# Kernel optimization log

Hardware: AMD Instinct MI355X
Metric: run time of the kernel (lower is better)

The kernel has to match this reference:

```python
import jax, jax.numpy as jnp
import numpy as np

N_NODES, N_EDGES, N_FEAT, N_HID = 50000, 800000, 512, 64


def gcn_conv(x, W, b, src, dst, ew):
    """PyG-style GCNConv: linear -> symmetric-normalized aggregation with self-loops -> +bias."""
    N = x.shape[0]
    h = x @ W  # [N, H]
    # degree includes the implicit self-loop of weight 1 (PyG gcn_norm default)
    deg = jax.ops.segment_sum(ew, dst, num_segments=N) + 1.0
    dinv = jax.lax.rsqrt(deg)  # deg^{-1/2}
    coef = dinv[src] * ew * dinv[dst]  # [E]
    out = jax.ops.segment_sum(h[src] * coef[:, None], dst, num_segments=N)
    out = out + h * (dinv * dinv)[:, None]  # self-loop contribution
    return out + b


def setup_inputs() -> dict:
    key = jax.random.key(0)
    k0, k1, k2, k3 = jax.random.split(key, 4)
    x = jax.random.normal(k0, (N_NODES, N_FEAT), dtype=jnp.float32)
    edge_index = jax.random.randint(k1, (2, N_EDGES), 0, N_NODES, dtype=jnp.int64)
    edge_weight = jnp.ones((N_EDGES,), dtype=jnp.float32)
    W1 = jax.random.normal(k2, (N_FEAT, N_HID), dtype=jnp.float32) * (1.0 / np.sqrt(N_FEAT))
    b1 = jnp.zeros((N_HID,), dtype=jnp.float32)
    W2 = jax.random.normal(k3, (N_HID, N_HID), dtype=jnp.float32) * (1.0 / np.sqrt(N_HID))
    b2 = jnp.zeros((N_HID,), dtype=jnp.float32)
    return {"x": x, "edge_index": edge_index, "edge_weight": edge_weight,
            "W1": W1, "b1": b1, "W2": W2, "b2": b2}


def reference(x, edge_index, edge_weight, W1, b1, W2, b2):
    # Grace.forward -> GCN_body.forward in eval mode (no dropout, no LN)
    src, dst = edge_index[0], edge_index[1]
    h = jax.nn.relu(gcn_conv(x, W1, b1, src, dst, edge_weight))
    h = jax.nn.relu(gcn_conv(h, W2, b2, src, dst, edge_weight))
    return h
```

## Files before the change

### kernel.cpp

```cpp
#include <hip/hip_runtime.h>
#include <hip/hip_bf16.h>

typedef __bf16 bf16x8 __attribute__((ext_vector_type(8)));
typedef float  f32x4  __attribute__((ext_vector_type(4)));

#define RNODES 64
#define ROWCAP 1792
#define NB 128
#define MAXNR 1024
#define FIXB 256

__device__ __forceinline__ float bf_lo(unsigned int v) { return __uint_as_float(v << 16); }
__device__ __forceinline__ float bf_hi(unsigned int v) { return __uint_as_float(v & 0xFFFF0000u); }

__device__ __forceinline__ void pack_one(const void* __restrict__ W, int f16,
                                         __hip_bfloat16* __restrict__ Wp, int K, int t) {
    int j  = t & 7;
    int l  = (t >> 3) & 63;
    int nt = (t >> 9) & 3;
    int kt = t >> 11;
    int k = kt * 32 + (l >> 4) * 8 + j;
    int n = nt * 16 + (l & 15);
    size_t gi = (size_t)k * 64 + n;
    Wp[t] = f16 ? ((const __hip_bfloat16*)W)[gi]
                : __float2bfloat16(((const float*)W)[gi]);
}

__global__ void setup_kernel(const unsigned int* __restrict__ ew_raw,
                             const unsigned int* __restrict__ ei_raw,
                             const void* __restrict__ W1, const void* __restrict__ W2,
                             int* __restrict__ flags,
                             __hip_bfloat16* __restrict__ W1p, __hip_bfloat16* __restrict__ W2p,
                             int F, int H) {
    int f16 = (ew_raw[0] == 0x3F803F80u) ? 1 : 0;
    if (blockIdx.x == 0 && threadIdx.x == 0) {
        flags[0] = f16;
        flags[1] = ((ei_raw[1] | ei_raw[3] | ei_raw[5] | ei_raw[7]) == 0u) ? 1 : 0;
        flags[2] = 0;
        flags[3] = 0;
        flags[4] = 1;
    }
    int t = blockIdx.x * 256 + threadIdx.x;
    if (t < F * 64)            pack_one(W1, f16, W1p, F, t);
    else if (t < (F + H) * 64) pack_one(W2, f16, W2p, H, t - F * 64);
}

__device__ __forceinline__ void gemm_body(const void* __restrict__ A,
                                          const __hip_bfloat16* __restrict__ Wp,
                                          int a_f32, __hip_bfloat16* __restrict__ out,
                                          int M, int K, int gt) {
    int wid  = gt >> 6;
    int lane = gt & 63;
    if (wid >= (M >> 4)) return;
    int row0 = wid << 4;
    int quad = lane >> 4, mr = lane & 15;
    const bf16x8* bp = (const bf16x8*)((const void*)Wp) + lane;

    f32x4 acc[4];
    #pragma unroll
    for (int nt = 0; nt < 4; ++nt) acc[nt] = (f32x4){0.f, 0.f, 0.f, 0.f};

    int KT = K >> 5;
    const __hip_bfloat16* ab    = (const __hip_bfloat16*)A + (size_t)(row0 + mr) * K + quad * 8;
    const float*          af32p = (const float*)A + (size_t)(row0 + mr) * K + quad * 8;

    int kt = 0;
    for (; kt + 8 <= KT; kt += 8) {
        bf16x8 af[8];
        if (a_f32) {
            #pragma unroll
            for (int u = 0; u < 8; ++u) {
                const float* ar = af32p + (kt + u) * 32;
                #pragma unroll
                for (int j = 0; j < 8; ++j) af[u][j] = (__bf16)ar[j];
            }
        } else {
            #pragma unroll
            for (int u = 0; u < 8; ++u)
                af[u] = ((const bf16x8*)((const void*)(ab + (kt + u) * 32)))[0];
        }
        #pragma unroll
        for (int u = 0; u < 8; ++u)
            #pragma unroll
            for (int nt = 0; nt < 4; ++nt)
                acc[nt] = __builtin_amdgcn_mfma_f32_16x16x32_bf16(
                              af[u], bp[((kt + u) * 4 + nt) * 64], acc[nt], 0, 0, 0);
    }
    for (; kt < KT; ++kt) {
        bf16x8 af;
        if (a_f32) {
            const float* ar = af32p + kt * 32;
            #pragma unroll
            for (int j = 0; j < 8; ++j) af[j] = (__bf16)ar[j];
        } else {
            af = ((const bf16x8*)((const void*)(ab + kt * 32)))[0];
        }
        #pragma unroll
        for (int nt = 0; nt < 4; ++nt)
            acc[nt] = __builtin_amdgcn_mfma_f32_16x16x32_bf16(
                          af, bp[(kt * 4 + nt) * 64], acc[nt], 0, 0, 0);
    }

    __hip_bfloat16* o = out + (size_t)row0 * 64;
    #pragma unroll
    for (int nt = 0; nt < 4; ++nt)
        #pragma unroll
        for (int rr = 0; rr < 4; ++rr)
            o[(size_t)(quad * 4 + rr) * 64 + nt * 16 + mr] = __float2bfloat16(acc[nt][rr]);
}

__global__ void gemm_mfma(const void* __restrict__ A, const __hip_bfloat16* __restrict__ Wp,
                          const int* __restrict__ flags, __hip_bfloat16* __restrict__ out,
                          int M, int K, int a_mode) {
    int gt = blockIdx.x * blockDim.x + threadIdx.x;
    int a_f32 = (a_mode == 2) && (flags[0] == 0);
    gemm_body(A, Wp, a_f32, out, M, K, gt);
}

__global__ void bgp1_kernel(const void* __restrict__ A, const __hip_bfloat16* __restrict__ Wp,
                            __hip_bfloat16* __restrict__ outH,
                            const int* __restrict__ ei, const void* __restrict__ ew,
                            int* __restrict__ flags,
                            int* __restrict__ blockhist, unsigned int* __restrict__ pkstage,
                            int M, int K, int E, int NR, int gblocks) {
    if ((int)blockIdx.x < gblocks) {
        gemm_body(A, Wp, flags[0] == 0, outH, M, K, blockIdx.x * 256 + threadIdx.x);
        return;
    }
    __shared__ int hist[MAXNR];
    int b = blockIdx.x - gblocks, tid = threadIdx.x;
    for (int i = tid; i < NR; i += 256) hist[i] = 0;
    __syncthreads();
    int f16 = flags[0], i64 = flags[1];

    int nw = f16 ? (E >> 1) : E;
    unsigned int expect = f16 ? 0x3F803F80u : 0x3F800000u;
    int wchunk = (nw + NB - 1) / NB;
    int w0 = b * wchunk, w1 = w0 + wchunk; if (w1 > nw) w1 = nw;
    const unsigned int* ewr = (const unsigned int*)ew;
    unsigned int bad = 0;
    for (int i = w0 + tid; i < w1; i += 256) bad |= (ewr[i] ^ expect);
    if (bad) flags[4] = 0;

    int chunk = (E + NB - 1) / NB;
    int e0 = b * chunk, e1 = e0 + chunk; if (e1 > E) e1 = E;
    for (int e = e0 + tid; e < e1; e += 256) {
        int s, d;
        if (i64) { s = ei[2LL * e]; d = ei[2LL * ((long long)E + e)]; }
        else     { s = ei[e];       d = ei[E + e]; }
        int r = d >> 6;
        atomicAdd(&hist[r], 1);
        pkstage[e] = ((unsigned int)r << 22) | ((unsigned int)s << 6) | (unsigned int)(d & 63);
    }
    __syncthreads();
    for (int i = tid; i < NR; i += 256) blockhist[b * NR + i] = hist[i];
}

__device__ __forceinline__ void check_body(const void* __restrict__ A, const void* __restrict__ W,
                                           int* __restrict__ flags,
                                           const __hip_bfloat16* __restrict__ out,
                                           int N, int K, int a_mode, int fidx, int bid) {
    __shared__ float xs[4 * 512];
    int f16 = flags[0];
    int a_f32 = (a_mode == 2) && (f16 == 0);
    int tid = threadIdx.x;
    int total = 4 * K;
    for (int t = tid; t < total; t += 256) {
        int nn = t / K, kk = t - nn * K;
        int n = (int)(((long long)(bid * 4 + nn) * 977) % N);
        long long gi = (long long)n * K + kk;
        float v = a_f32 ? (float)(__bf16)(((const float*)A)[gi])
                        : __bfloat162float(((const __hip_bfloat16*)A)[gi]);
        xs[t] = v;
    }
    __syncthreads();
    int j = tid & 63, local = tid >> 6;
    int n = (int)(((long long)(bid * 4 + local) * 977) % N);
    const float* xr = xs + local * K;
    float acc = 0.f;
    if (f16) {
        const __hip_bfloat16* Wb = (const __hip_bfloat16*)W;
        #pragma unroll 8
        for (int k = 0; k < K; ++k) acc += xr[k] * __bfloat162float(Wb[(long long)k * 64 + j]);
    } else {
        const float* Wf = (const float*)W;
        #pragma unroll 8
        for (int k = 0; k < K; ++k) acc += xr[k] * (float)(__bf16)(Wf[(long long)k * 64 + j]);
    }
    float d = __bfloat162float(out[(size_t)n * 64 + j]) - acc;
    if (!(fabsf(d) <= 0.05f)) atomicAdd(&flags[fidx], 1);
}

__device__ __forceinline__ void fix_body(const void* __restrict__ A, const void* __restrict__ W,
                                         const int* __restrict__ flags,
                                         __hip_bfloat16* __restrict__ out,
                                         int N, int K, int a_mode, int fidx,
                                         int bid, int nblocks) {
    if (flags[fidx] == 0) return;
    __shared__ float xs[4 * 512];
    int tid = threadIdx.x;
    int f16 = flags[0];
    int a_f32 = (a_mode == 2) && (f16 == 0);
    int total = 4 * K;
    for (int node0 = bid * 4; node0 < N; node0 += nblocks * 4) {
        __syncthreads();
        for (int t = tid; t < total; t += 256) {
            int nn = t / K, kk = t - nn * K;
            if (node0 + nn < N) {
                long long gi = (long long)(node0 + nn) * K + kk;
                xs[t] = a_f32 ? ((const float*)A)[gi]
                              : __bfloat162float(((const __hip_bfloat16*)A)[gi]);
            }
        }
        __syncthreads();
        int j = tid & 63, local = tid >> 6;
        int n = node0 + local;
        if (n < N) {
            const float* xr = xs + local * K;
            float acc = 0.f;
            if (f16) {
                const __hip_bfloat16* Wb = (const __hip_bfloat16*)W;
                #pragma unroll 8
                for (int k = 0; k < K; ++k) acc += xr[k] * __bfloat162float(Wb[(long long)k * 64 + j]);
            } else {
                const float* Wf = (const float*)W;
                #pragma unroll 8
                for (int k = 0; k < K; ++k) acc += xr[k] * Wf[(long long)k * 64 + j];
            }
            out[(long long)n * 64 + j] = __float2bfloat16(acc);
        }
    }
}

__global__ void p2chk_kernel(int* __restrict__ blockhist, int* __restrict__ rtot, int NR,
                             const void* __restrict__ A, const void* __restrict__ W,
                             int* __restrict__ flags, const __hip_bfloat16* __restrict__ out,
                             int N, int K, int a_mode, int fidx, int p2b) {
    if ((int)blockIdx.x < p2b) {
        int r    = blockIdx.x * 4 + (threadIdx.x >> 6);
        int lane = threadIdx.x & 63;
        if (r < NR) {
            int b0 = lane * 2;
            int c0 = blockhist[(size_t)b0 * NR + r];
            int c1 = blockhist[(size_t)(b0 + 1) * NR + r];
            int s = c0 + c1;
            int incl = s;
            #pragma unroll
            for (int off = 1; off < 64; off <<= 1) {
                int t = __shfl_up(incl, off, 64);
                if (lane >= off) incl += t;
            }
            int run = r * ROWCAP + (incl - s);
            blockhist[(size_t)b0 * NR + r]       = run;
            blockhist[(size_t)(b0 + 1) * NR + r] = run + c0;
            if (lane == 63) rtot[r] = incl > ROWCAP ? ROWCAP : incl;
        }
    } else {
        check_body(A, W, flags, out, N, K, a_mode, fidx, blockIdx.x - p2b);
    }
}

__global__ void p3fix_kernel(const int* __restrict__ blockhist,
                             const unsigned int* __restrict__ pkstage,
                             const void* __restrict__ ew, const int* __restrict__ flags,
                             unsigned int* __restrict__ sortedR, float* __restrict__ sortedRW,
                             int E, int NR,
                             const void* __restrict__ A, const void* __restrict__ W,
                             __hip_bfloat16* __restrict__ out,
                             int N, int K, int a_mode, int fidx) {
    if ((int)blockIdx.x < NB) {
        __shared__ int loff[MAXNR];
        int b = blockIdx.x, tid = threadIdx.x;
        for (int i = tid; i < NR; i += 256) loff[i] = blockhist[b * NR + i];
        __syncthreads();
        int chunk = (E + NB - 1) / NB;
        int e0 = b * chunk, e1 = e0 + chunk; if (e1 > E) e1 = E;
        int ones = flags[4], f16 = flags[0];
        for (int e = e0 + tid; e < e1; e += 256) {
            unsigned int pk = pkstage[e];
            int r = (int)(pk >> 22);
            int pos = atomicAdd(&loff[r], 1);
            if (pos < (r + 1) * ROWCAP) {
                sortedR[pos] = pk;
                if (!ones) {
                    float w = f16 ? __bfloat162float(((const __hip_bfloat16*)ew)[e])
                                  : ((const float*)ew)[e];
                    sortedRW[pos] = w;
                }
            }
        }
    } else {
        fix_body(A, W, flags, out, N, K, a_mode, fidx, blockIdx.x - NB, FIXB);
    }
}

__global__ void range_kernel(const unsigned int* __restrict__ sortedR,
                             const float* __restrict__ sortedRW,
                             const int* __restrict__ rtot, const int* __restrict__ flags,
                             int* __restrict__ cnt, float* __restrict__ dinv,
                             int* __restrict__ row_ptr,
                             int* __restrict__ sortedS, float* __restrict__ sortedW, int N) {
    __shared__ unsigned int sd[ROWCAP];
    __shared__ float sw[ROWCAP];
    __shared__ int   cnt0[RNODES], pref[RNODES], slot[RNODES];
    __shared__ float wsum[RNODES];

    int r   = blockIdx.x;
    int tid = threadIdx.x;
    int ones = flags[4];
    int T = rtot[r];

    if (tid < RNODES) { cnt0[tid] = 0; wsum[tid] = 0.f; }
    __syncthreads();

    size_t g = (size_t)r * ROWCAP;
    for (int t = tid; t < T; t += 256) {
        sd[t] = sortedR[g + t];
        if (!ones) sw[t] = sortedRW[g + t];
    }
    __syncthreads();

    for (int k = tid; k < T; k += 256) {
        int dl = sd[k] & (RNODES - 1);
        atomicAdd(&cnt0[dl], 1);
        if (!ones) atomicAdd(&wsum[dl], sw[k]);
    }
    __syncthreads();

    if (tid < RNODES) pref[tid] = cnt0[tid];
    __syncthreads();
    for (int off = 1; off < RNODES; off <<= 1) {
        int v = (tid < RNODES && tid >= off) ? pref[tid - off] : 0;
        __syncthreads();
        if (tid < RNODES) pref[tid] += v;
        __syncthreads();
    }
    if (tid < RNODES) {
        int excl = pref[tid] - cnt0[tid];
        int n = r * RNODES + tid;
        slot[tid] = r * ROWCAP + excl;
        if (n < N) {
            cnt[n]     = cnt0[tid];
            row_ptr[n] = r * ROWCAP + excl;
            float wd = ones ? (float)cnt0[tid] : wsum[tid];
            dinv[n]  = rsqrtf(wd + 1.0f);
        }
    }
    __syncthreads();

    for (int k = tid; k < T; k += 256) {
        unsigned int v = sd[k];
        int dl = v & (RNODES - 1);
        int p = atomicAdd(&slot[dl], 1);
        sortedS[p] = (int)((v >> 6) & 0xFFFFu);
        if (!ones) sortedW[p] = sw[k];
    }
}

__global__ void check_fast(const void* __restrict__ A, const void* __restrict__ W,
                           int* __restrict__ flags, const __hip_bfloat16* __restrict__ out,
                           int N, int K, int a_mode, int fidx) {
    check_body(A, W, flags, out, N, K, a_mode, fidx, blockIdx.x);
}

__global__ void gemm_fix(const void* __restrict__ A, const void* __restrict__ W,
                         const int* __restrict__ flags, __hip_bfloat16* __restrict__ out,
                         int N, int K, int a_mode, int fidx) {
    fix_body(A, W, flags, out, N, K, a_mode, fidx, blockIdx.x, FIXB);
}

__global__ void gather_kernel(const __hip_bfloat16* __restrict__ h,
                              const int* __restrict__ sortedS, const float* __restrict__ sortedW,
                              const int* __restrict__ cnt, const int* __restrict__ row_ptr,
                              const float* __restrict__ dinv,
                              const void* __restrict__ bias, const int* __restrict__ flags,
                              void* __restrict__ out, int internal, int N) {
    int gt = blockIdx.x * blockDim.x + threadIdx.x;
    int n = gt >> 5, jl = gt & 31;
    if (n >= N) return;
    int f16 = flags[0], ones = flags[4];
    float dn = dinv[n];
    int deg = cnt[n];
    int base = row_ptr[n];
    const int*   p  = sortedS + base;
    const float* pw = sortedW + base;
    const unsigned int* h32 = (const unsigned int*)h;
    float a0 = 0.f, a1 = 0.f;
    int s = 0;
    for (; s + 4 <= deg; s += 4) {
        int s0 = p[s], s1 = p[s + 1], s2 = p[s + 2], s3 = p[s + 3];
        float c0 = dinv[s0] * dn, c1 = dinv[s1] * dn;
        float c2 = dinv[s2] * dn, c3 = dinv[s3] * dn;
        if (!ones) { c0 *= pw[s]; c1 *= pw[s + 1]; c2 *= pw[s + 2]; c3 *= pw[s + 3]; }
        unsigned int v0 = h32[(size_t)s0 * 32 + jl];
        unsigned int v1 = h32[(size_t)s1 * 32 + jl];
        unsigned int v2 = h32[(size_t)s2 * 32 + jl];
        unsigned int v3 = h32[(size_t)s3 * 32 + jl];
        a0 += c0 * bf_lo(v0) + c1 * bf_lo(v1) + c2 * bf_lo(v2) + c3 * bf_lo(v3);
        a1 += c0 * bf_hi(v0) + c1 * bf_hi(v1) + c2 * bf_hi(v2) + c3 * bf_hi(v3);
    }
    for (; s < deg; ++s) {
        int s0 = p[s];
        float c = dinv[s0] * dn;
        if (!ones) c *= pw[s];
        unsigned int v = h32[(size_t)s0 * 32 + jl];
        a0 += c * bf_lo(v);
        a1 += c * bf_hi(v);
    }
    unsigned int vs = h32[(size_t)n * 32 + jl];
    float dn2 = dn * dn;
    a0 += dn2 * bf_lo(vs);
    a1 += dn2 * bf_hi(vs);
    if (f16) {
        unsigned int bv = ((const unsigned int*)bias)[jl];
        a0 += bf_lo(bv);
        a1 += bf_hi(bv);
    } else {
        a0 += ((const float*)bias)[jl * 2];
        a1 += ((const float*)bias)[jl * 2 + 1];
    }
    a0 = fmaxf(a0, 0.f);
    a1 = fmaxf(a1, 0.f);
    if (internal | f16) {
        __hip_bfloat16 b0 = __float2bfloat16(a0), b1 = __float2bfloat16(a1);
        unsigned int pack = ((unsigned int)(*(unsigned short*)&b1) << 16)
                          | (unsigned int)(*(unsigned short*)&b0);
        ((unsigned int*)out)[(size_t)n * 32 + jl] = pack;
    } else {
        ((float*)out)[(size_t)n * 64 + jl * 2]     = a0;
        ((float*)out)[(size_t)n * 64 + jl * 2 + 1] = a1;
    }
}

extern "C" void kernel_launch(void* const* d_in, const int* in_sizes, int n_in,
                              void* d_out, int out_size, void* d_ws, size_t ws_size,
                              hipStream_t stream) {
    const void* x  = d_in[0];
    const int*  ei = (const int*)d_in[1];
    const void* ew = d_in[2];
    const void* W1 = d_in[3];
    const void* b1 = d_in[4];
    const void* W2 = d_in[5];
    const void* b2 = d_in[6];

    const int H = in_sizes[4];
    const int F = in_sizes[3] / H;
    const int N = in_sizes[0] / F;
    const int E = in_sizes[1] / 2;

    const int NR = (N + RNODES - 1) / RNODES;

    char* w = (char*)d_ws;
    size_t off = 0;
    auto alloc = [&](size_t bytes) {
        char* r = w + off;
        off += (bytes + 255) & ~(size_t)255;
        return r;
    };
    int*   flags     = (int*)alloc(32);
    int*   blockhist = (int*)alloc((size_t)NB * NR * 4);
    int*   rtot      = (int*)alloc((size_t)NR * 4);
    int*   cnt       = (int*)alloc((size_t)N * 4);
    float* dinv      = (float*)alloc((size_t)N * 4);
    int*   row_ptr   = (int*)alloc((size_t)N * 4);
    unsigned int* pkstage = (unsigned int*)alloc((size_t)E * 4);
    unsigned int* sortedR = (unsigned int*)alloc((size_t)NR * ROWCAP * 4);
    float* sortedRW  = (float*)alloc((size_t)NR * ROWCAP * 4);
    int*   sortedS   = (int*)alloc((size_t)NR * ROWCAP * 4);
    float* sortedW   = (float*)alloc((size_t)NR * ROWCAP * 4);
    __hip_bfloat16* bufH = (__hip_bfloat16*)alloc((size_t)N * 64 * 2);
    __hip_bfloat16* bufR = (__hip_bfloat16*)alloc((size_t)N * 64 * 2);
    __hip_bfloat16* W1p  = (__hip_bfloat16*)alloc((size_t)F * 64 * 2);
    __hip_bfloat16* W2p  = (__hip_bfloat16*)alloc((size_t)H * 64 * 2);

    int gblocks = ((N / 16) * 64 + 255) / 256;
    int p2b = (NR + 3) / 4;

    setup_kernel<<<((F + H) * 64 + 255) / 256, 256, 0, stream>>>(
        (const unsigned int*)ew, (const unsigned int*)ei, W1, W2, flags, W1p, W2p, F, H);

    bgp1_kernel<<<gblocks + NB, 256, 0, stream>>>(x, W1p, bufH, ei, ew, flags,
                                                  blockhist, pkstage,
                                                  N, F, E, NR, gblocks);

    p2chk_kernel<<<p2b + 64, 256, 0, stream>>>(blockhist, rtot, NR,
                                               x, W1, flags, bufH, N, F, 2, 2, p2b);

    p3fix_kernel<<<NB + FIXB, 256, 0, stream>>>(blockhist, pkstage, ew, flags,
                                                sortedR, sortedRW, E, NR,
                                                x, W1, bufH, N, F, 2, 2);

    range_kernel<<<NR, 256, 0, stream>>>(sortedR, sortedRW, rtot, flags,
                                         cnt, dinv, row_ptr, sortedS, sortedW, N);

    gather_kernel<<<(N * 32 + 255) / 256, 256, 0, stream>>>(bufH, sortedS, sortedW,
                                                            cnt, row_ptr, dinv,
                                                            b1, flags, bufR, 1, N);
    gemm_mfma<<<gblocks, 256, 0, stream>>>(bufR, W2p, flags, bufH, N, H, 0);
    check_fast<<<64, 256, 0, stream>>>(bufR, W2, flags, bufH, N, H, 0, 3);
    gemm_fix<<<FIXB, 256, 0, stream>>>(bufR, W2, flags, bufH, N, H, 0, 3);

    gather_kernel<<<(N * 32 + 255) / 256, 256, 0, stream>>>(bufH, sortedS, sortedW,
                                                            cnt, row_ptr, dinv,
                                                            b2, flags, d_out, 0, N);
}
```

Measured before the change: 310.4 us.

## Fuse layer-1 gather with layer-2 GEMM and overlap check with second gather

The first aggregation now writes its 16-node tile to shared memory and immediately runs the 64x64 MFMA projection, removing the separate GEMM launch and its reread of the intermediate. The correctness check on the second GEMM runs in the same launch as the second gather, speculatively. A regather kernel reruns aggregation only if the fix path flagged corrections. This cuts launches and memory traffic but adds a block-level sync and an extra buffer.

```diff
diff --git a/kernel.cpp b/kernel.cpp
--- a/kernel.cpp
+++ b/kernel.cpp
@@ -107,14 +107,6 @@
         #pragma unroll
         for (int rr = 0; rr < 4; ++rr)
             o[(size_t)(quad * 4 + rr) * 64 + nt * 16 + mr] = __float2bfloat16(acc[nt][rr]);
-}
-
-__global__ void gemm_mfma(const void* __restrict__ A, const __hip_bfloat16* __restrict__ Wp,
-                          const int* __restrict__ flags, __hip_bfloat16* __restrict__ out,
-                          int M, int K, int a_mode) {
-    int gt = blockIdx.x * blockDim.x + threadIdx.x;
-    int a_f32 = (a_mode == 2) && (flags[0] == 0);
-    gemm_body(A, Wp, a_f32, out, M, K, gt);
 }
 
 __global__ void bgp1_kernel(const void* __restrict__ A, const __hip_bfloat16* __restrict__ Wp,
@@ -357,34 +349,20 @@
     }
 }
 
-__global__ void check_fast(const void* __restrict__ A, const void* __restrict__ W,
-                           int* __restrict__ flags, const __hip_bfloat16* __restrict__ out,
-                           int N, int K, int a_mode, int fidx) {
-    check_body(A, W, flags, out, N, K, a_mode, fidx, blockIdx.x);
-}
-
-__global__ void gemm_fix(const void* __restrict__ A, const void* __restrict__ W,
-                         const int* __restrict__ flags, __hip_bfloat16* __restrict__ out,
-                         int N, int K, int a_mode, int fidx) {
-    fix_body(A, W, flags, out, N, K, a_mode, fidx, blockIdx.x, FIXB);
-}
-
-__global__ void gather_kernel(const __hip_bfloat16* __restrict__ h,
-                              const int* __restrict__ sortedS, const float* __restrict__ sortedW,
-                              const int* __restrict__ cnt, const int* __restrict__ row_ptr,
-                              const float* __restrict__ dinv,
-                              const void* __restrict__ bias, const int* __restrict__ flags,
-                              void* __restrict__ out, int internal, int N) {
-    int gt = blockIdx.x * blockDim.x + threadIdx.x;
-    int n = gt >> 5, jl = gt & 31;
-    if (n >= N) return;
-    int f16 = flags[0], ones = flags[4];
+__device__ __forceinline__ unsigned int gather_pair(const unsigned int* __restrict__ h32,
+                                                    const int* __restrict__ sortedS,
+                                                    const float* __restrict__ sortedW,
+                                                    const int* __restrict__ cnt,
+                                                    const int* __restrict__ row_ptr,
+                                                    const float* __restrict__ dinv,
+                                                    const void* __restrict__ bias,
+                                                    int f16, int ones, int n, int jl,
+                                                    float* f0, float* f1) {
     float dn = dinv[n];
     int deg = cnt[n];
     int base = row_ptr[n];
     const int*   p  = sortedS + base;
     const float* pw = sortedW + base;
-    const unsigned int* h32 = (const unsigned int*)h;
     float a0 = 0.f, a1 = 0.f;
     int s = 0;
     for (; s + 4 <= deg; s += 4) {
@@ -421,14 +399,115 @@
     }
     a0 = fmaxf(a0, 0.f);
     a1 = fmaxf(a1, 0.f);
-    if (internal | f16) {
-        __hip_bfloat16 b0 = __float2bfloat16(a0), b1 = __float2bfloat16(a1);
-        unsigned int pack = ((unsigned int)(*(unsigned short*)&b1) << 16)
-                          | (unsigned int)(*(unsigned short*)&b0);
-        ((unsigned int*)out)[(size_t)n * 32 + jl] = pack;
+    *f0 = a0; *f1 = a1;
+    __hip_bfloat16 b0 = __float2bfloat16(a0), b1 = __float2bfloat16(a1);
+    return ((unsigned int)(*(unsigned short*)&b1) << 16) | (unsigned int)(*(unsigned short*)&b0);
+}
+
+__global__ void g1g2_kernel(const __hip_bfloat16* __restrict__ h,
+                            const int* __restrict__ sortedS, const float* __restrict__ sortedW,
+                            const int* __restrict__ cnt, const int* __restrict__ row_ptr,
+                            const float* __restrict__ dinv,
+                            const void* __restrict__ bias, const __hip_bfloat16* __restrict__ Wp,
+                            const int* __restrict__ flags,
+                            __hip_bfloat16* __restrict__ bufR, __hip_bfloat16* __restrict__ outH2,
+                            int N) {
+    __shared__ unsigned int aT[16 * 32];
+    int f16 = flags[0], ones = flags[4];
+    const unsigned int* h32 = (const unsigned int*)h;
+    int node0 = blockIdx.x * 16;
+
+    #pragma unroll
+    for (int it = 0; it < 2; ++it) {
+        int slot = it * 256 + threadIdx.x;
+        int nl = slot >> 5, jl = slot & 31;
+        int n = node0 + nl;
+        if (n < N) {
+            float f0, f1;
+            unsigned int pack = gather_pair(h32, sortedS, sortedW, cnt, row_ptr, dinv,
+                                            bias, f16, ones, n, jl, &f0, &f1);
+            aT[nl * 32 + jl] = pack;
+            ((unsigned int*)bufR)[(size_t)n * 32 + jl] = pack;
+        }
+    }
+    __syncthreads();
+
+    if (threadIdx.x < 64 && node0 < N) {
+        int lane = threadIdx.x;
+        int quad = lane >> 4, mr = lane & 15;
+        const bf16x8* bp = (const bf16x8*)((const void*)Wp) + lane;
+        f32x4 acc[4];
+        #pragma unroll
+        for (int nt = 0; nt < 4; ++nt) acc[nt] = (f32x4){0.f, 0.f, 0.f, 0.f};
+        #pragma unroll
+        for (int kt = 0; kt < 2; ++kt) {
+            bf16x8 af = ((const bf16x8*)((const void*)aT))[mr * 8 + quad + kt * 4];
+            #pragma unroll
+            for (int nt = 0; nt < 4; ++nt)
+                acc[nt] = __builtin_amdgcn_mfma_f32_16x16x32_bf16(
+                              af, bp[(kt * 4 + nt) * 64], acc[nt], 0, 0, 0);
+        }
+        __hip_bfloat16* o = outH2 + (size_t)node0 * 64;
+        #pragma unroll
+        for (int nt = 0; nt < 4; ++nt)
+            #pragma unroll
+            for (int rr = 0; rr < 4; ++rr)
+                if (node0 + quad * 4 + rr < N)
+                    o[(size_t)(quad * 4 + rr) * 64 + nt * 16 + mr] = __float2bfloat16(acc[nt][rr]);
+    }
+}
+
+__global__ void g2chk_kernel(const __hip_bfloat16* __restrict__ h2,
+                             const int* __restrict__ sortedS, const float* __restrict__ sortedW,
+                             const int* __restrict__ cnt, const int* __restrict__ row_ptr,
+                             const float* __restrict__ dinv,
+                             const void* __restrict__ bias, int* __restrict__ flags,
+                             const void* __restrict__ bufR, const void* __restrict__ W2,
+                             void* __restrict__ out, int N, int K, int gb2) {
+    if ((int)blockIdx.x < gb2) {
+        int gt = blockIdx.x * 256 + threadIdx.x;
+        if (gt >= N * 32) return;
+        int n = gt >> 5, jl = gt & 31;
+        int f16 = flags[0], ones = flags[4];
+        float f0, f1;
+        unsigned int pack = gather_pair((const unsigned int*)h2, sortedS, sortedW, cnt,
+                                        row_ptr, dinv, bias, f16, ones, n, jl, &f0, &f1);
+        if (f16) {
+            ((unsigned int*)out)[(size_t)n * 32 + jl] = pack;
+        } else {
+            ((float*)out)[(size_t)n * 64 + jl * 2]     = f0;
+            ((float*)out)[(size_t)n * 64 + jl * 2 + 1] = f1;
+        }
     } else {
-        ((float*)out)[(size_t)n * 64 + jl * 2]     = a0;
-        ((float*)out)[(size_t)n * 64 + jl * 2 + 1] = a1;
+        check_body(bufR, W2, flags, h2, N, K, 0, 3, blockIdx.x - gb2);
+    }
+}
+
+__global__ void gemm_fix(const void* __restrict__ A, const void* __restrict__ W,
+                         const int* __restrict__ flags, __hip_bfloat16* __restrict__ out,
+                         int N, int K, int a_mode, int fidx) {
+    fix_body(A, W, flags, out, N, K, a_mode, fidx, blockIdx.x, FIXB);
+}
+
+__global__ void regather_kernel(const __hip_bfloat16* __restrict__ h2,
+                                const int* __restrict__ sortedS, const float* __restrict__ sortedW,
+                                const int* __restrict__ cnt, const int* __restrict__ row_ptr,
+                                const float* __restrict__ dinv,
+                                const void* __restrict__ bias, const int* __restrict__ flags,
+                                void* __restrict__ out, int N) {
+    if (flags[3] == 0) return;
+    int f16 = flags[0], ones = flags[4];
+    for (int gt = blockIdx.x * 256 + threadIdx.x; gt < N * 32; gt += FIXB * 256) {
+        int n = gt >> 5, jl = gt & 31;
+        float f0, f1;
+        unsigned int pack = gather_pair((const unsigned int*)h2, sortedS, sortedW, cnt,
+                                        row_ptr, dinv, bias, f16, ones, n, jl, &f0, &f1);
+        if (f16) {
+            ((unsigned int*)out)[(size_t)n * 32 + jl] = pack;
+        } else {
+            ((float*)out)[(size_t)n * 64 + jl * 2]     = f0;
+            ((float*)out)[(size_t)n * 64 + jl * 2 + 1] = f1;
+        }
     }
 }
 
@@ -468,13 +547,16 @@
     float* sortedRW  = (float*)alloc((size_t)NR * ROWCAP * 4);
     int*   sortedS   = (int*)alloc((size_t)NR * ROWCAP * 4);
     float* sortedW   = (float*)alloc((size_t)NR * ROWCAP * 4);
-    __hip_bfloat16* bufH = (__hip_bfloat16*)alloc((size_t)N * 64 * 2);
-    __hip_bfloat16* bufR = (__hip_bfloat16*)alloc((size_t)N * 64 * 2);
-    __hip_bfloat16* W1p  = (__hip_bfloat16*)alloc((size_t)F * 64 * 2);
-    __hip_bfloat16* W2p  = (__hip_bfloat16*)alloc((size_t)H * 64 * 2);
+    __hip_bfloat16* bufH  = (__hip_bfloat16*)alloc((size_t)N * 64 * 2);
+    __hip_bfloat16* bufR  = (__hip_bfloat16*)alloc((size_t)N * 64 * 2);
+    __hip_bfloat16* bufH2 = (__hip_bfloat16*)alloc((size_t)N * 64 * 2);
+    __hip_bfloat16* W1p   = (__hip_bfloat16*)alloc((size_t)F * 64 * 2);
+    __hip_bfloat16* W2p   = (__hip_bfloat16*)alloc((size_t)H * 64 * 2);
 
     int gblocks = ((N / 16) * 64 + 255) / 256;
     int p2b = (NR + 3) / 4;
+    int tblocks = (N + 15) / 16;
+    int gb2 = (N * 32 + 255) / 256;
 
     setup_kernel<<<((F + H) * 64 + 255) / 256, 256, 0, stream>>>(
         (const unsigned int*)ew, (const unsigned int*)ei, W1, W2, flags, W1p, W2p, F, H);
@@ -493,14 +575,13 @@
     range_kernel<<<NR, 256, 0, stream>>>(sortedR, sortedRW, rtot, flags,
                                          cnt, dinv, row_ptr, sortedS, sortedW, N);
 
-    gather_kernel<<<(N * 32 + 255) / 256, 256, 0, stream>>>(bufH, sortedS, sortedW,
-                                                            cnt, row_ptr, dinv,
-                                                            b1, flags, bufR, 1, N);
-    gemm_mfma<<<gblocks, 256, 0, stream>>>(bufR, W2p, flags, bufH, N, H, 0);
-    check_fast<<<64, 256, 0, stream>>>(bufR, W2, flags, bufH, N, H, 0, 3);
-    gemm_fix<<<FIXB, 256, 0, stream>>>(bufR, W2, flags, bufH, N, H, 0, 3);
-
-    gather_kernel<<<(N * 32 + 255) / 256, 256, 0, stream>>>(bufH, sortedS, sortedW,
-                                                            cnt, row_ptr, dinv,
-                                                            b2, flags, d_out, 0, N);
-}
+    g1g2_kernel<<<tblocks, 256, 0, stream>>>(bufH, sortedS, sortedW, cnt, row_ptr, dinv,
+                                             b1, W2p, flags, bufR, bufH2, N);
+
+    g2chk_kernel<<<gb2 + 64, 256, 0, stream>>>(bufH2, sortedS, sortedW, cnt, row_ptr, dinv,
+                                               b2, flags, bufR, W2, d_out, N, H, gb2);
+
+    gemm_fix<<<FIXB, 256, 0, stream>>>(bufR, W2, flags, bufH2, N, H, 0, 3);
+    regather_kernel<<<FIXB, 256, 0, stream>>>(bufH2, sortedS, sortedW, cnt, row_ptr, dinv,
+                                              b2, flags, d_out, N);
+}
```

New measurement: 301.8 us. -2.8%, faster.
